# Kernel tuning notes

Hardware: AMD Instinct MI355X
Metric: run time of the kernel (lower is better)

## Reference

```python
import jax, jax.numpy as jnp
import numpy as np

B, LR_DIM, G_DIM, K, D, T = 256, 1024, 512, 64, 256, 8
GRID = jnp.linspace(-4.0, 4.0, 41)  # registered buffer in torch module


def _mu_bell(x, c, a_bell, b_bell):
    # generalized bell membership, clamp(a,b) >= 1e-3 as in torch
    a = jnp.maximum(a_bell, 1e-3)
    b = jnp.maximum(b_bell, 1e-3)
    return 1.0 / (1.0 + jnp.abs((x - c) / a) ** (2.0 * b))


def _mu_s(x, a, b):
    eps = 1e-12
    a2 = jnp.minimum(a, b)
    b2 = jnp.maximum(a, b)
    mid = (a2 + b2) * 0.5
    up = 2.0 * ((x - a2) / (b2 - a2 + eps)) ** 2
    dn = 1.0 - 2.0 * ((b2 - x) / (b2 - a2 + eps)) ** 2
    y = jnp.where((x > a2) & (x <= mid), up, jnp.zeros_like(x))
    y = jnp.where((x > mid) & (x <= b2), dn, y)
    return jnp.where(x > b2, jnp.ones_like(x), y)


def _fuzzify(x, a_bell, b_bell):
    # x: (B,d) -> (B,2d)
    xs = 4.0 * jnp.tanh(x / 4.0)
    xb = _mu_bell(xs, 0.0, a_bell, b_bell)
    xS = _mu_s(xs, -1.0, 1.0)
    return jnp.concatenate([xb, xS], axis=-1)


def _defuzzify(rt, a_bell, b_bell):
    # rt: (B,2d) -> centroid (B,d)
    d = rt.shape[1] // 2
    rb, rs = rt[:, :d], rt[:, d:]
    g = GRID[None, None, :]                      # (1,1,G)
    c_b = 4.0 * jnp.tanh(rb)[..., None]          # (B,d,1)
    c_s = 4.0 * jnp.tanh(rs)[..., None]
    mu_b = _mu_bell(g, c_b, a_bell, b_bell)      # (B,d,G)
    a_s = jnp.clip(c_s - 1.0, -4.0, 4.0)
    b_s = jnp.clip(c_s + 1.0, -4.0, 4.0)
    mu_s = _mu_s(g, a_s, b_s)
    cen_b = (g * mu_b).sum(-1) / (mu_b.sum(-1) + 1e-12)
    cen_s = (g * mu_s).sum(-1) / (mu_s.sum(-1) + 1e-12)
    return 0.5 * cen_b + 0.5 * cen_s


def _forward(wsi_lr, genomics, FT, W_lr, b_lr, W_g, b_g, WqI, WqG, WkI, WkG,
             WvI, WvG, mlp_W1, mlp_b1, mlp_W2, mlp_b2, Wf, bf, Wi, bi, Vf, Vi,
             a_bell, b_bell):
    scale = jnp.float32(D) ** 0.5
    lr = wsi_lr @ W_lr + b_lr                    # (B,d)
    g = genomics @ W_g + b_g
    lr_f = _fuzzify(lr, a_bell, b_bell)          # (B,2d)
    g_f = _fuzzify(g, a_bell, b_bell)
    QI = lr_f @ WqI                              # (B,d), loop-invariant
    QG = g_f @ WqG
    Ft0 = jnp.broadcast_to(FT[None], (wsi_lr.shape[0],) + FT.shape)  # (B,K,d)

    def step(Ft, _):
        sI = jnp.einsum('bd,bkd->bk', QI, Ft @ WkI) / scale
        sG = jnp.einsum('bd,bkd->bk', QG, Ft @ WkG) / scale
        rtI = jnp.einsum('bk,bke->be', jax.nn.softmax(sI, axis=-1), Ft @ WvI)  # (B,2d)
        rtG = jnp.einsum('bk,bke->be', jax.nn.softmax(sG, axis=-1), Ft @ WvG)
        r = 0.5 * _defuzzify(rtI, a_bell, b_bell) + 0.5 * _defuzzify(rtG, a_bell, b_bell)
        rb = jnp.broadcast_to(r[:, None, :], Ft.shape)              # (B,K,d)
        x = Ft + rb
        F_tilde = jax.nn.gelu(x @ mlp_W1 + mlp_b1, approximate=False) @ mlp_W2 + mlp_b2 + x
        f_gate = jax.nn.sigmoid(rb @ Wf + bf + jnp.tanh(Ft @ Vf))
        i_gate = jax.nn.sigmoid(rb @ Wi + bi + jnp.tanh(Ft @ Vi))
        Ft_new = f_gate * Ft + i_gate * jnp.tanh(F_tilde)
        return Ft_new, Ft_new

    _, steps = jax.lax.scan(step, Ft0, None, length=T)
    # torch stores step `T-s` result at index s-1: list index 0 holds the LAST
    # computed state, index T-1 the first -> reverse chronological order
    return steps[::-1]  # (T,B,K,d)


def setup_inputs() -> dict:
    key = jax.random.key(0)
    ks = jax.random.split(key, 20)

    def rn(k, shape, scale):
        return jax.random.normal(k, shape, dtype=jnp.float32) * scale

    z = lambda *s: jnp.zeros(s, jnp.float32)
    return dict(
        wsi_lr=rn(ks[0], (B, LR_DIM), 1.0),
        genomics=rn(ks[1], (B, G_DIM), 1.0),
        FT=rn(ks[2], (K, D), 0.02),
        W_lr=rn(ks[3], (LR_DIM, D), LR_DIM ** -0.5), b_lr=z(D),
        W_g=rn(ks[4], (G_DIM, D), G_DIM ** -0.5), b_g=z(D),
        WqI=rn(ks[5], (2 * D, D), (2 * D) ** -0.5),
        WqG=rn(ks[6], (2 * D, D), (2 * D) ** -0.5),
        WkI=rn(ks[7], (D, D), D ** -0.5),
        WkG=rn(ks[8], (D, D), D ** -0.5),
        WvI=rn(ks[9], (D, 2 * D), D ** -0.5),
        WvG=rn(ks[10], (D, 2 * D), D ** -0.5),
        mlp_W1=rn(ks[11], (D, 2 * D), D ** -0.5), mlp_b1=z(2 * D),
        mlp_W2=rn(ks[12], (2 * D, D), (2 * D) ** -0.5), mlp_b2=z(D),
        Wf=rn(ks[13], (D, D), D ** -0.5), bf=z(D),
        Wi=rn(ks[14], (D, D), D ** -0.5), bi=z(D),
        Vf=rn(ks[15], (D, D), D ** -0.5),
        Vi=rn(ks[16], (D, D), D ** -0.5),
        a_bell=jnp.float32(1.0),
        b_bell=jnp.float32(2.0),
    )


def reference(wsi_lr, genomics, FT, W_lr, b_lr, W_g, b_g, WqI, WqG, WkI, WkG,
              WvI, WvG, mlp_W1, mlp_b1, mlp_W2, mlp_b2, Wf, bf, Wi, bi, Vf, Vi,
              a_bell, b_bell):
    return _forward(wsi_lr, genomics, FT, W_lr, b_lr, W_g, b_g, WqI, WqG, WkI,
                    WkG, WvI, WvG, mlp_W1, mlp_b1, mlp_W2, mlp_b2, Wf, bf, Wi,
                    bi, Vf, Vi, a_bell, b_bell)
```

## Files before the change

### kernel.cpp

```cpp
#include <hip/hip_runtime.h>
#include <hip/hip_bf16.h>

#define B_    256
#define K_    64
#define D_    256
#define T_    8
#define NROW  (B_*K_)

typedef short short8v __attribute__((ext_vector_type(8)));
typedef float f32x4  __attribute__((ext_vector_type(4)));

__device__ __forceinline__ float fexp2(float x) { return __builtin_amdgcn_exp2f(x); }
__device__ __forceinline__ float flog2(float x) { return __builtin_amdgcn_logf(x); }

__device__ __forceinline__ float sigmoid_f(float x) {
  return 1.f / (1.f + fexp2(x * -1.4426950408889634f));
}
__device__ __forceinline__ float tanh_fast(float x) {
  float xc = fminf(fmaxf(x, -30.f), 30.f);
  float t = fexp2(xc * 2.8853900817779268f);
  return (t - 1.f) / (t + 1.f);
}
__device__ __forceinline__ float gelu_f(float x) {
  return 0.5f * x * (1.f + erff(x * 0.70710678118654752440f));
// ... 9 lines not shown
  float mid = 0.5f * (a2 + b2);
  float inv = 1.f / (b2 - a2 + 1e-12f);
  if (x > b2)  return 1.f;
  if (x > mid) { float u = (b2 - x) * inv; return 1.f - 2.f * u * u; }
  if (x > a2)  { float u = (x - a2) * inv; return 2.f * u * u; }
  return 0.f;
}
__device__ __forceinline__ float pow_abs(float z, float e2b) {
  return fexp2(e2b * flog2(fabsf(z)));
}
__device__ __forceinline__ float defuzz_one(float rb_, float rs_, float ab, float bb) {
  float e2b = 2.f * bb;
  float inv_ab = 1.f / ab;
  float cb = 4.f * tanh_fast(rb_);
  float num = 0.f, den = 0.f;
  #pragma unroll
  for (int j = 0; j < 41; ++j) {
    float gj = -4.f + 0.2f * (float)j;
    float mu = 1.f / (1.f + pow_abs((gj - cb) * inv_ab, e2b));
    num += gj * mu; den += mu;
  }
  float cenb = num / (den + 1e-12f);
  float cs = 4.f * tanh_fast(rs_);
  float as_ = fminf(fmaxf(cs - 1.f, -4.f), 4.f);
  float bs_ = fminf(fmaxf(cs + 1.f, -4.f), 4.f);
  num = 0.f; den = 0.f;
  {
    float mid = 0.5f * (as_ + bs_);
    float inv = 1.f / (bs_ - as_ + 1e-12f);
    #pragma unroll
    for (int j = 0; j < 41; ++j) {
      float gj = -4.f + 0.2f * (float)j;
      float mu;
      if (gj > bs_)      mu = 1.f;
      else if (gj > mid) { float u = (bs_ - gj) * inv; mu = 1.f - 2.f * u * u; }
      else if (gj > as_) { float u = (gj - as_) * inv; mu = 2.f * u * u; }
      else               mu = 0.f;
      num += gj * mu; den += mu;
    }
  }
  float cens = num / (den + 1e-12f);
  return 0.5f * cenb + 0.5f * cens;
}

__global__ __launch_bounds__(256) void k_convert(
    const float* __restrict__ W1, const float* __restrict__ Vf, const float* __restrict__ Vi,
    const float* __restrict__ W2, const float* __restrict__ FT,
    const float* __restrict__ WkI, const float* __restrict__ WkG,
    const float* __restrict__ WvI, const float* __restrict__ WvG,
    const float* __restrict__ Wf,  const float* __restrict__ Wi,
    unsigned short* __restrict__ B1t, unsigned short* __restrict__ W2t,
    unsigned short* __restrict__ FTbf,
    float* __restrict__ WkIt, float* __restrict__ WkGt,
    unsigned short* __restrict__ Wv2, unsigned short* __restrict__ WB)
{
  int idx = blockIdx.x * 256 + threadIdx.x;
  if (idx < 262144) {
    int n = idx >> 8, k = idx & 255;
    float v = (n < 512) ? W1[(size_t)k*512 + n]
            : (n < 768) ? Vf[(size_t)k*256 + (n-512)]
                        : Vi[(size_t)k*256 + (n-768)];
    B1t[idx] = f2bf(v);
  } else if (idx < 393216) {
    int j = idx - 262144;
    int n = j >> 9, k = j & 511;
    W2t[j] = f2bf(W2[(size_t)k*256 + n]);
  } else if (idx < 409600) {
    int j = idx - 393216;
    FTbf[j] = f2bf(FT[j]);
  } else if (idx < 475136) {
    int j = idx - 409600;
    int k = j >> 8, n = j & 255;
    WkIt[j] = WkI[(size_t)n*256 + k];
  } else if (idx < 540672) {
    int j = idx - 475136;
    int k = j >> 8, n = j & 255;
    WkGt[j] = WkG[(size_t)n*256 + k];
  } else if (idx < 802816) {
    int j = idx - 540672;
    int d = j >> 10, c = j & 1023;
    float v = (c < 512) ? WvI[(size_t)d*512 + c] : WvG[(size_t)d*512 + (c-512)];
    Wv2[j] = f2bf(v);
  } else if (idx < 1064960) {
    int j = idx - 802816;
    int d = j >> 10, c = j & 1023;
    float v = (c < 512) ? W1[(size_t)d*512 + c]
            : (c < 768) ? Wf[(size_t)d*256 + (c-512)]
                        : Wi[(size_t)d*256 + (c-768)];
    WB[j] = f2bf(v);
  }
}

__global__ __launch_bounds__(256) void k_pre_lin(
    const float* __restrict__ wsi, const float* __restrict__ gen,
    const float* __restrict__ W_lr, const float* __restrict__ b_lr,
    const float* __restrict__ W_g,  const float* __restrict__ b_g,
    const float* __restrict__ a_p,  const float* __restrict__ b_p,
    float* __restrict__ lrf, float* __restrict__ gf)
{
  int g_ix = blockIdx.x;
  int half = g_ix >> 4, tile = g_ix & 15;
  int bx = tile & 3, by = tile >> 2;
  int n0 = bx * 64, m0 = by * 64;
  const float* A    = half ? gen  : wsi;
  const float* Bm   = half ? W_g  : W_lr;
  const float* bias = half ? b_g  : b_lr;
  float* outp       = half ? gf   : lrf;
  int KK            = half ? 512  : 1024;
  float ab = fmaxf(a_p[0], 0.001f), bb = fmaxf(b_p[0], 0.001f);
  float e2b = 2.f * bb, inv_ab = 1.f / ab;

  __shared__ float As[16][64];
  __shared__ float Bs[16][64];
  int tid = threadIdx.x, tx = tid & 15, ty = tid >> 4;
  float acc[4][4] = {};
  int am = tid >> 2, ak = (tid & 3) * 4;
  int bk = tid >> 4, bn = (tid & 15) * 4;
  const float* arow = A + (size_t)(m0 + am) * KK;
  for (int k0 = 0; k0 < KK; k0 += 16) {
    float4 av = *(const float4*)(arow + k0 + ak);
    As[ak+0][am] = av.x; As[ak+1][am] = av.y; As[ak+2][am] = av.z; As[ak+3][am] = av.w;
    *(float4*)&Bs[bk][bn] = *(const float4*)(Bm + (size_t)(k0 + bk) * 256 + n0 + bn);
    __syncthreads();
    #pragma unroll
    for (int kk = 0; kk < 16; ++kk) {
      float a0 = As[kk][ty*4+0], a1 = As[kk][ty*4+1], a2 = As[kk][ty*4+2], a3 = As[kk][ty*4+3];
      float b0 = Bs[kk][tx*4+0], b1 = Bs[kk][tx*4+1], b2 = Bs[kk][tx*4+2], b3 = Bs[kk][tx*4+3];
      acc[0][0]=fmaf(a0,b0,acc[0][0]); acc[0][1]=fmaf(a0,b1,acc[0][1]); acc[0][2]=fmaf(a0,b2,acc[0][2]); acc[0][3]=fmaf(a0,b3,acc[0][3]);
      acc[1][0]=fmaf(a1,b0,acc[1][0]); acc[1][1]=fmaf(a1,b1,acc[1][1]); acc[1][2]=fmaf(a1,b2,acc[1][2]); acc[1][3]=fmaf(a1,b3,acc[1][3]);
      acc[2][0]=fmaf(a2,b0,acc[2][0]); acc[2][1]=fmaf(a2,b1,acc[2][1]); acc[2][2]=fmaf(a2,b2,acc[2][2]); acc[2][3]=fmaf(a2,b3,acc[2][3]);
      acc[3][0]=fmaf(a3,b0,acc[3][0]); acc[3][1]=fmaf(a3,b1,acc[3][1]); acc[3][2]=fmaf(a3,b2,acc[3][2]); acc[3][3]=fmaf(a3,b3,acc[3][3]);
    }
    __syncthreads();
  }
  #pragma unroll
  for (int i = 0; i < 4; ++i) {
    int row = m0 + ty*4 + i;
    #pragma unroll
    for (int j = 0; j < 4; ++j) {
      int col = n0 + tx*4 + j;
      float v = acc[i][j] + bias[col];
      float xs = 4.f * tanh_fast(v * 0.25f);
// ... 39 lines not shown
    }
    __syncthreads();
  }
  #pragma unroll
  for (int i = 0; i < 4; ++i) {
    float4 v = make_float4(acc[i][0], acc[i][1], acc[i][2], acc[i][3]);
    *(float4*)(outp + (size_t)(m0 + ty*4 + i) * 256 + n0 + tx*4) = v;
  }
}

__global__ __launch_bounds__(256) void k_pre_qp(
    const float* __restrict__ QI, const float* __restrict__ QG,
    const float* __restrict__ WkIt, const float* __restrict__ WkGt,
    float* __restrict__ qIp, float* __restrict__ qGp)
{
  int g_ix = blockIdx.x;
  int half = g_ix >> 4, tile = g_ix & 15;
  int bx = tile & 3, by = tile >> 2;
  int n0 = bx * 64, m0 = by * 64;
  const float* A  = half ? QG   : QI;
  const float* Bm = half ? WkGt : WkIt;
  float* outp     = half ? qGp  : qIp;

  __shared__ float As[16][64];
  __shared__ float Bs[16][64];
  int tid = threadIdx.x, tx = tid & 15, ty = tid >> 4;
  float acc[4][4] = {};
  int am = tid >> 2, ak = (tid & 3) * 4;
  int bk = tid >> 4, bn = (tid & 15) * 4;
  const float* arow = A + (size_t)(m0 + am) * 256;
  for (int k0 = 0; k0 < 256; k0 += 16) {
    float4 av = *(const float4*)(arow + k0 + ak);
    As[ak+0][am] = av.x; As[ak+1][am] = av.y; As[ak+2][am] = av.z; As[ak+3][am] = av.w;
    *(float4*)&Bs[bk][bn] = *(const float4*)(Bm + (size_t)(k0 + bk) * 256 + n0 + bn);
    __syncthreads();
    #pragma unroll
    for (int kk = 0; kk < 16; ++kk) {
      float a0 = As[kk][ty*4+0], a1 = As[kk][ty*4+1], a2 = As[kk][ty*4+2], a3 = As[kk][ty*4+3];
      float b0 = Bs[kk][tx*4+0], b1 = Bs[kk][tx*4+1], b2 = Bs[kk][tx*4+2], b3 = Bs[kk][tx*4+3];
      acc[0][0]=fmaf(a0,b0,acc[0][0]); acc[0][1]=fmaf(a0,b1,acc[0][1]); acc[0][2]=fmaf(a0,b2,acc[0][2]); acc[0][3]=fmaf(a0,b3,acc[0][3]);
      acc[1][0]=fmaf(a1,b0,acc[1][0]); acc[1][1]=fmaf(a1,b1,acc[1][1]); acc[1][2]=fmaf(a1,b2,acc[1][2]); acc[1][3]=fmaf(a1,b3,acc[1][3]);
      acc[2][0]=fmaf(a2,b0,acc[2][0]); acc[2][1]=fmaf(a2,b1,acc[2][1]); acc[2][2]=fmaf(a2,b2,acc[2][2]); acc[2][3]=fmaf(a2,b3,acc[2][3]);
      acc[3][0]=fmaf(a3,b0,acc[3][0]); acc[3][1]=fmaf(a3,b1,acc[3][1]); acc[3][2]=fmaf(a3,b2,acc[3][2]); acc[3][3]=fmaf(a3,b3,acc[3][3]);
    }
    __syncthreads();
  }
  #pragma unroll
  for (int i = 0; i < 4; ++i) {
    float4 v = make_float4(acc[i][0], acc[i][1], acc[i][2], acc[i][3]);
    *(float4*)(outp + (size_t)(m0 + ty*4 + i) * 256 + n0 + tx*4) = v;
  }
}

__global__ __launch_bounds__(512) void k_scan(
    const unsigned short* __restrict__ FTbf, const float* __restrict__ FTf,
    const float* __restrict__ qIp, const float* __restrict__ qGp,
    const unsigned short* __restrict__ Wv2, const unsigned short* __restrict__ WB,
    const float* __restrict__ b1, const float* __restrict__ bfv,
    const float* __restrict__ biv, const float* __restrict__ b2,
    const unsigned short* __restrict__ B1t, const unsigned short* __restrict__ W2t,
    const float* __restrict__ a_p, const float* __restrict__ b_p,
    unsigned short* __restrict__ Gf, unsigned short* __restrict__ Gi,
    float* __restrict__ out)
{
  __shared__ __align__(16) short Fs[64*264];
  __shared__ __align__(16) short Bstage[64*264];
  __shared__ __align__(16) short Wstage[256*72];
  __shared__ __align__(16) short A2ch[64*72];
  __shared__ float qv[512];
  __shared__ float red[512];
  __shared__ float prl[128];
  __shared__ float ftb[512];
  __shared__ float rL[256];
  __shared__ float rWall[1024];

  int b = blockIdx.x, tid = threadIdx.x;
  int w = tid >> 6, lane = tid & 63, lr = lane & 15, lh = lane >> 4;
  int rg = w & 3, cg = w >> 2;
  float ab = fmaxf(a_p[0], 0.001f), bb = fmaxf(b_p[0], 0.001f);

  #pragma unroll
  for (int p = 0; p < 4; ++p) {
    int idx = (p*512 + tid) * 8;
    int row = idx >> 8, col = idx & 255;
    *(float4*)&Fs[row*264 + col] = *(const float4*)&FTbf[idx];
  }
  qv[tid] = (tid < 256) ? qIp[(size_t)b*256 + tid] : qGp[(size_t)b*256 + tid - 256];
  __syncthreads();

  const float* Fprev = nullptr;
  for (int st = 0; st < T_; ++st) {
    float* Fout = out + (size_t)(7 - st) * NROW * 256;

    {
      int which = tid >> 8, tt = tid & 255, k = tt & 63, part = tt >> 6;
      const unsigned int* frow = (const unsigned int*)&Fs[k*264 + part*64];
      const float* q0 = qv + which*256 + part*64;
      float s0 = 0.f;
      #pragma unroll
      for (int d2 = 0; d2 < 32; ++d2) {
        unsigned int pr = frow[d2];
        float f0 = __uint_as_float(pr << 16);
        float f1 = __uint_as_float(pr & 0xffff0000u);
        s0 = fmaf(f1, q0[2*d2+1], fmaf(f0, q0[2*d2], s0));
      }
      red[which*256 + tt] = s0;
    }
    __syncthreads();
    if (tid < 128) {
      int which = tid >> 6, kk = tid & 63;
      const float* rp = red + which*256;
      float s = (rp[kk] + rp[64+kk] + rp[128+kk] + rp[192+kk]) * (1.f/16.f);
      float m = s;
      for (int off = 32; off; off >>= 1) m = fmaxf(m, __shfl_xor(m, off, 64));
      float e = fexp2((s - m) * 1.4426950408889634f);
      float sum = e;
      for (int off = 32; off; off >>= 1) sum += __shfl_xor(sum, off, 64);
      prl[which*64 + kk] = e / sum;
    }
    __syncthreads();
    {
      int which = tid >> 8, tt = tid & 255;
      const float* pp = prl + which*64;
      float f0 = 0.f;
      #pragma unroll 8
      for (int kk = 0; kk < 64; ++kk)
        f0 = fmaf(pp[kk], bfss((unsigned short)Fs[kk*264 + tt]), f0);
      ftb[which*256 + tt] = f0;
    }
    __syncthreads();
    {
      int half = tid >> 8, tt = tid & 255;
      const float* fb = ftb + half*256;
      const unsigned short* wv = Wv2 + half*512 + tt;
      float a0 = 0.f, a1 = 0.f;
      #pragma unroll 4
      for (int d = 0; d < 256; ++d) {
        float fv = fb[d];
        a0 = fmaf(fv, bfss(wv[(size_t)d*1024]),       a0);
        a1 = fmaf(fv, bfss(wv[(size_t)d*1024 + 256]), a1);
      }
      red[half*256 + tt] = defuzz_one(a0, a1, ab, bb);
    }
    __syncthreads();
    if (tid < 256) rL[tid] = 0.5f * (red[tid] + red[256 + tid]);
    __syncthreads();
    {
      float w0 = 0.f, w1 = 0.f;
      const unsigned short* wb0 = WB + tid;
      #pragma unroll 4
      for (int d = 0; d < 256; ++d) {
        float rv = rL[d];
        w0 = fmaf(rv, bfss(wb0[(size_t)d*1024]),       w0);
        w1 = fmaf(rv, bfss(wb0[(size_t)d*1024 + 512]), w1);
      }
      rWall[tid]       = w0 + b1[tid];
      rWall[512 + tid] = w1 + ((tid < 256) ? bfv[tid] : biv[tid - 256]);
    }
    __syncthreads();

    for (int c = 8; c < 16; ++c) {
      #pragma unroll
      for (int p = 0; p < 4; ++p) {
        int idx = (p*512 + tid) * 8;
        int row = idx >> 8, col = idx & 255;
        *(float4*)&Bstage[row*264 + col] = *(const float4*)&B1t[(size_t)c*16384 + idx];
      }
      __syncthreads();
      #pragma unroll
      for (int f = 0; f < 2; ++f) {
        f32x4 acc = {0.f,0.f,0.f,0.f};
        int nb = cg*32 + f*16;
        #pragma unroll
        for (int ks = 0; ks < 8; ++ks) {
          short8v av = *(const short8v*)&Fs[(rg*16 + lr)*264 + ks*32 + lh*8];
          short8v bv = *(const short8v*)&Bstage[(nb + lr)*264 + ks*32 + lh*8];
          acc = __builtin_amdgcn_mfma_f32_16x16x32_bf16(av, bv, acc, 0, 0, 0);
        }
        int gc = c*64 + nb + lr;
        float add = rWall[gc];
        int cc = gc - 512;
        #pragma unroll
        for (int r = 0; r < 4; ++r) {
          int row = b*64 + rg*16 + lh*4 + r;
          unsigned short val = f2bf(sigmoid_f(add + tanh_fast(acc[r])));
          if (cc < 256) Gf[(size_t)row*256 + cc]       = val;
          else          Gi[(size_t)row*256 + cc - 256] = val;
        }
      }
      __syncthreads();
    }

    f32x4 O[8];
    #pragma unroll
    for (int nn = 0; nn < 8; ++nn) { O[nn][0]=0.f; O[nn][1]=0.f; O[nn][2]=0.f; O[nn][3]=0.f; }
    for (int c = 0; c < 8; ++c) {
      #pragma unroll
      for (int p = 0; p < 4; ++p) {
        int idx = (p*512 + tid) * 8;
        int row = idx >> 8, col = idx & 255;
        *(float4*)&Bstage[row*264 + col] = *(const float4*)&B1t[(size_t)c*16384 + idx];
      }
      #pragma unroll
      for (int p = 0; p < 4; ++p) {
        int idx = (p*512 + tid) * 8;
        int n = idx >> 6, kk = idx & 63;
        *(float4*)&Wstage[n*72 + kk] = *(const float4*)&W2t[(size_t)n*512 + c*64 + kk];
      }
      __syncthreads();
      #pragma unroll
      for (int f = 0; f < 2; ++f) {
        f32x4 acc = {0.f,0.f,0.f,0.f};
        int nb = cg*32 + f*16;
        #pragma unroll
        for (int ks = 0; ks < 8; ++ks) {
          short8v av = *(const short8v*)&Fs[(rg*16 + lr)*264 + ks*32 + lh*8];
          short8v bv = *(const short8v*)&Bstage[(nb + lr)*264 + ks*32 + lh*8];
          acc = __builtin_amdgcn_mfma_f32_16x16x32_bf16(av, bv, acc, 0, 0, 0);
        }
        int gc = c*64 + nb + lr;
        float add = rWall[gc];
        #pragma unroll
        for (int r = 0; r < 4; ++r)
          A2ch[(rg*16 + lh*4 + r)*72 + nb + lr] = f2bf(gelu_f(acc[r] + add));
      }
      __syncthreads();
      #pragma unroll
      for (int ks2 = 0; ks2 < 2; ++ks2) {
        short8v av = *(const short8v*)&A2ch[(rg*16 + lr)*72 + ks2*32 + lh*8];
        #pragma unroll
        for (int nn = 0; nn < 8; ++nn) {
          short8v bv = *(const short8v*)&Wstage[(cg*128 + nn*16 + lr)*72 + ks2*32 + lh*8];
          O[nn] = __builtin_amdgcn_mfma_f32_16x16x32_bf16(av, bv, O[nn], 0, 0, 0);
        }
      }
      __syncthreads();
    }

    #pragma unroll
    for (int nn = 0; nn < 8; ++nn) {
      int col = cg*128 + nn*16 + lr;
      float b2c = b2[col], rv = rL[col];
      #pragma unroll
      for (int r = 0; r < 4; ++r) {
        int rowl = rg*16 + lh*4 + r;
        int row = b*64 + rowl;
        float Ftv = (st == 0) ? FTf[rowl*256 + col] : Fprev[(size_t)row*256 + col];
        float ftld = O[nn][r] + b2c + Ftv + rv;
        float fg = bfss(Gf[(size_t)row*256 + col]);
        float ig = bfss(Gi[(size_t)row*256 + col]);
        float ov = fg * Ftv + ig * tanh_fast(ftld);
        Fout[(size_t)row*256 + col] = ov;
        Fs[rowl*264 + col] = f2bf(ov);
      }
    }
    Fprev = Fout;
    __syncthreads();
  }
}

extern "C" void kernel_launch(void* const* d_in, const int* in_sizes, int n_in,
                              void* d_out, int out_size, void* d_ws, size_t ws_size,
                              hipStream_t stream)
{
  (void)in_sizes; (void)n_in; (void)out_size; (void)ws_size;
  const float* wsi  = (const float*)d_in[0];
  const float* gen  = (const float*)d_in[1];
  const float* FT   = (const float*)d_in[2];
  const float* W_lr = (const float*)d_in[3];
  const float* b_lr = (const float*)d_in[4];
  const float* W_g  = (const float*)d_in[5];
  const float* b_g  = (const float*)d_in[6];
  const float* WqI  = (const float*)d_in[7];
  const float* WqG  = (const float*)d_in[8];
  const float* WkI  = (const float*)d_in[9];
  const float* WkG  = (const float*)d_in[10];
  const float* WvI  = (const float*)d_in[11];
  const float* WvG  = (const float*)d_in[12];
  const float* W1   = (const float*)d_in[13];
  const float* b1   = (const float*)d_in[14];
  const float* W2   = (const float*)d_in[15];
  const float* b2   = (const float*)d_in[16];
  const float* Wf   = (const float*)d_in[17];
  const float* bf   = (const float*)d_in[18];
  const float* Wi   = (const float*)d_in[19];
  const float* bi   = (const float*)d_in[20];
  const float* Vf   = (const float*)d_in[21];
  const float* Vi   = (const float*)d_in[22];
  const float* a_p  = (const float*)d_in[23];
  const float* b_p  = (const float*)d_in[24];

  float* out = (float*)d_out;
  float* ws  = (float*)d_ws;
  float* qIp   = ws;
  float* qGp   = qIp   + 65536;
  float* lrf   = qGp   + 65536;
  float* gf    = lrf   + 131072;
  float* QI    = gf    + 131072;
  float* QG    = QI    + 65536;
  float* WkIt  = QG    + 65536;
  float* WkGt  = WkIt  + 65536;
  unsigned short* Gfb  = (unsigned short*)(WkGt + 65536);
  unsigned short* Gib  = Gfb  + 4194304;
  unsigned short* FTbf = Gib  + 4194304;
  unsigned short* B1t  = FTbf + 16384;
  unsigned short* W2t  = B1t  + 262144;
  unsigned short* Wv2  = W2t  + 131072;
  unsigned short* WB   = Wv2  + 262144;

  k_convert<<<4160, 256, 0, stream>>>(W1, Vf, Vi, W2, FT, WkI, WkG, WvI, WvG, Wf, Wi,
                                      B1t, W2t, FTbf, WkIt, WkGt, Wv2, WB);
  k_pre_lin<<<32, 256, 0, stream>>>(wsi, gen, W_lr, b_lr, W_g, b_g, a_p, b_p, lrf, gf);
  k_pre_q<<<32, 256, 0, stream>>>(lrf, gf, WqI, WqG, QI, QG);
  k_pre_qp<<<32, 256, 0, stream>>>(QI, QG, WkIt, WkGt, qIp, qGp);

  k_scan<<<256, 512, 0, stream>>>(FTbf, FT, qIp, qGp, Wv2, WB,
                                  b1, bf, bi, b2, B1t, W2t, a_p, b_p,
                                  Gfb, Gib, out);
}
```

Measured before the change: 870.3 us.

## Move scan matvecs onto MFMA with split-bf16 and drop LDS weight staging

The per-step score dot products and the Wv/WB matrix-vector products in the scan kernel now run on bf16 MFMA instead of scalar FMA loops. The vector operands and the weights are split into hi/lo bf16 pairs so the products keep near-fp32 accuracy. The B1t/W2t operands are read straight from global memory instead of being staged through shared memory, which removes several barriers and shrinks LDS use so more blocks can be resident (launch bounds ask for 4 per CU). The costs are wasted MFMA lanes (most columns or rows are zero or discarded), three MFMAs per split-precision product, and uncoalesced global fragment loads that now depend on L2 hits.

```diff
diff --git a/kernel.cpp b/kernel.cpp
--- a/kernel.cpp
+++ b/kernel.cpp
@@ -85,7 +85,8 @@
     unsigned short* __restrict__ B1t, unsigned short* __restrict__ W2t,
     unsigned short* __restrict__ FTbf,
     float* __restrict__ WkIt, float* __restrict__ WkGt,
-    unsigned short* __restrict__ Wv2, unsigned short* __restrict__ WB)
+    unsigned short* __restrict__ Wv2tH, unsigned short* __restrict__ Wv2tL,
+    unsigned short* __restrict__ WBtH,  unsigned short* __restrict__ WBtL)
 {
   int idx = blockIdx.x * 256 + threadIdx.x;
   if (idx < 262144) {
@@ -111,16 +112,20 @@
     WkGt[j] = WkG[(size_t)n*256 + k];
   } else if (idx < 802816) {
     int j = idx - 540672;
-    int d = j >> 10, c = j & 1023;
-    float v = (c < 512) ? WvI[(size_t)d*512 + c] : WvG[(size_t)d*512 + (c-512)];
-    Wv2[j] = f2bf(v);
+    int n = j >> 8, d = j & 255;
+    float v = (n < 512) ? WvI[(size_t)d*512 + n] : WvG[(size_t)d*512 + (n-512)];
+    unsigned short hi = f2bf(v);
+    Wv2tH[j] = hi;
+    Wv2tL[j] = f2bf(v - bfss(hi));
   } else if (idx < 1064960) {
     int j = idx - 802816;
-    int d = j >> 10, c = j & 1023;
-    float v = (c < 512) ? W1[(size_t)d*512 + c]
-            : (c < 768) ? Wf[(size_t)d*256 + (c-512)]
-                        : Wi[(size_t)d*256 + (c-768)];
-    WB[j] = f2bf(v);
+    int n = j >> 8, d = j & 255;
+    float v = (n < 512) ? W1[(size_t)d*512 + n]
+            : (n < 768) ? Wf[(size_t)d*256 + (n-512)]
+                        : Wi[(size_t)d*256 + (n-768)];
+    unsigned short hi = f2bf(v);
+    WBtH[j] = hi;
+    WBtL[j] = f2bf(v - bfss(hi));
   }
 }
 
@@ -266,10 +271,11 @@
   }
 }
 
-__global__ __launch_bounds__(512) void k_scan(
+__global__ __launch_bounds__(512, 4) void k_scan(
     const unsigned short* __restrict__ FTbf, const float* __restrict__ FTf,
     const float* __restrict__ qIp, const float* __restrict__ qGp,
-    const unsigned short* __restrict__ Wv2, const unsigned short* __restrict__ WB,
+    const unsigned short* __restrict__ Wv2tH, const unsigned short* __restrict__ Wv2tL,
+    const unsigned short* __restrict__ WBtH,  const unsigned short* __restrict__ WBtL,
     const float* __restrict__ b1, const float* __restrict__ bfv,
     const float* __restrict__ biv, const float* __restrict__ b2,
     const unsigned short* __restrict__ B1t, const unsigned short* __restrict__ W2t,
@@ -278,20 +284,24 @@
     float* __restrict__ out)
 {
   __shared__ __align__(16) short Fs[64*264];
-  __shared__ __align__(16) short Bstage[64*264];
-  __shared__ __align__(16) short Wstage[256*72];
   __shared__ __align__(16) short A2ch[64*72];
-  __shared__ float qv[512];
+  __shared__ __align__(16) short qpack[4*256];
+  __shared__ __align__(16) short ftbhH[512];
+  __shared__ __align__(16) short ftbhL[512];
+  __shared__ __align__(16) short rLhH[256];
+  __shared__ __align__(16) short rLhL[256];
+  __shared__ float sctmp[4*64];
   __shared__ float red[512];
   __shared__ float prl[128];
-  __shared__ float ftb[512];
   __shared__ float rL[256];
+  __shared__ float rtbuf[1024];
   __shared__ float rWall[1024];
 
   int b = blockIdx.x, tid = threadIdx.x;
   int w = tid >> 6, lane = tid & 63, lr = lane & 15, lh = lane >> 4;
   int rg = w & 3, cg = w >> 2;
   float ab = fmaxf(a_p[0], 0.001f), bb = fmaxf(b_p[0], 0.001f);
+  short8v zfrag = {0,0,0,0,0,0,0,0};
 
   #pragma unroll
   for (int p = 0; p < 4; ++p) {
@@ -299,32 +309,37 @@
     int row = idx >> 8, col = idx & 255;
     *(float4*)&Fs[row*264 + col] = *(const float4*)&FTbf[idx];
   }
-  qv[tid] = (tid < 256) ? qIp[(size_t)b*256 + tid] : qGp[(size_t)b*256 + tid - 256];
+  {
+    int which = tid >> 8, tt = tid & 255;
+    float v = which ? qGp[(size_t)b*256 + tt] : qIp[(size_t)b*256 + tt];
+    unsigned short hi = f2bf(v);
+    qpack[which*256 + tt]       = hi;
+    qpack[(which+2)*256 + tt]   = f2bf(v - bfss(hi));
+  }
   __syncthreads();
 
   const float* Fprev = nullptr;
   for (int st = 0; st < T_; ++st) {
     float* Fout = out + (size_t)(7 - st) * NROW * 256;
 
-    {
-      int which = tid >> 8, tt = tid & 255, k = tt & 63, part = tt >> 6;
-      const unsigned int* frow = (const unsigned int*)&Fs[k*264 + part*64];
-      const float* q0 = qv + which*256 + part*64;
-      float s0 = 0.f;
-      #pragma unroll
-      for (int d2 = 0; d2 < 32; ++d2) {
-        unsigned int pr = frow[d2];
-        float f0 = __uint_as_float(pr << 16);
-        float f1 = __uint_as_float(pr & 0xffff0000u);
-        s0 = fmaf(f1, q0[2*d2+1], fmaf(f0, q0[2*d2], s0));
-      }
-      red[which*256 + tt] = s0;
+    if (w < 4) {
+      f32x4 acc = {0.f,0.f,0.f,0.f};
+      #pragma unroll
+      for (int ks = 0; ks < 8; ++ks) {
+        short8v av = *(const short8v*)&Fs[(rg*16 + lr)*264 + ks*32 + lh*8];
+        short8v bq = (lr < 4) ? *(const short8v*)&qpack[lr*256 + ks*32 + lh*8] : zfrag;
+        acc = __builtin_amdgcn_mfma_f32_16x16x32_bf16(av, bq, acc, 0, 0, 0);
+      }
+      if (lr < 4) {
+        #pragma unroll
+        for (int r = 0; r < 4; ++r)
+          sctmp[lr*64 + rg*16 + lh*4 + r] = acc[r];
+      }
     }
     __syncthreads();
     if (tid < 128) {
       int which = tid >> 6, kk = tid & 63;
-      const float* rp = red + which*256;
-      float s = (rp[kk] + rp[64+kk] + rp[128+kk] + rp[192+kk]) * (1.f/16.f);
+      float s = (sctmp[which*64 + kk] + sctmp[(which+2)*64 + kk]) * (1.f/16.f);
       float m = s;
       for (int off = 32; off; off >>= 1) m = fmaxf(m, __shfl_xor(m, off, 64));
       float e = fexp2((s - m) * 1.4426950408889634f);
@@ -340,47 +355,67 @@
       #pragma unroll 8
       for (int kk = 0; kk < 64; ++kk)
         f0 = fmaf(pp[kk], bfss((unsigned short)Fs[kk*264 + tt]), f0);
-      ftb[which*256 + tt] = f0;
+      unsigned short hi = f2bf(f0);
+      ftbhH[which*256 + tt] = hi;
+      ftbhL[which*256 + tt] = f2bf(f0 - bfss(hi));
+    }
+    __syncthreads();
+    #pragma unroll
+    for (int i = 0; i < 8; ++i) {
+      int n0 = (w*8 + i) * 16;
+      int aoff = (n0 < 512) ? 0 : 256;
+      f32x4 acc = {0.f,0.f,0.f,0.f};
+      #pragma unroll
+      for (int ks = 0; ks < 8; ++ks) {
+        short8v ah = *(const short8v*)&ftbhH[aoff + ks*32 + lh*8];
+        short8v al = *(const short8v*)&ftbhL[aoff + ks*32 + lh*8];
+        short8v bh = *(const short8v*)&Wv2tH[(size_t)(n0 + lr)*256 + ks*32 + lh*8];
+        short8v bl = *(const short8v*)&Wv2tL[(size_t)(n0 + lr)*256 + ks*32 + lh*8];
+        acc = __builtin_amdgcn_mfma_f32_16x16x32_bf16(ah, bh, acc, 0, 0, 0);
+        acc = __builtin_amdgcn_mfma_f32_16x16x32_bf16(al, bh, acc, 0, 0, 0);
+        acc = __builtin_amdgcn_mfma_f32_16x16x32_bf16(ah, bl, acc, 0, 0, 0);
+      }
+      if (lh == 0) rtbuf[n0 + lr] = acc[0];
     }
     __syncthreads();
     {
       int half = tid >> 8, tt = tid & 255;
-      const float* fb = ftb + half*256;
-      const unsigned short* wv = Wv2 + half*512 + tt;
-      float a0 = 0.f, a1 = 0.f;
-      #pragma unroll 4
-      for (int d = 0; d < 256; ++d) {
-        float fv = fb[d];
-        a0 = fmaf(fv, bfss(wv[(size_t)d*1024]),       a0);
-        a1 = fmaf(fv, bfss(wv[(size_t)d*1024 + 256]), a1);
-      }
-      red[half*256 + tt] = defuzz_one(a0, a1, ab, bb);
-    }
-    __syncthreads();
-    if (tid < 256) rL[tid] = 0.5f * (red[tid] + red[256 + tid]);
+      red[half*256 + tt] = defuzz_one(rtbuf[half*512 + tt], rtbuf[half*512 + 256 + tt], ab, bb);
+    }
+    __syncthreads();
+    if (tid < 256) {
+      float rv = 0.5f * (red[tid] + red[256 + tid]);
+      rL[tid] = rv;
+      unsigned short hi = f2bf(rv);
+      rLhH[tid] = hi;
+      rLhL[tid] = f2bf(rv - bfss(hi));
+    }
+    __syncthreads();
+    #pragma unroll
+    for (int i = 0; i < 8; ++i) {
+      int n0 = (w*8 + i) * 16;
+      f32x4 acc = {0.f,0.f,0.f,0.f};
+      #pragma unroll
+      for (int ks = 0; ks < 8; ++ks) {
+        short8v ah = *(const short8v*)&rLhH[ks*32 + lh*8];
+        short8v al = *(const short8v*)&rLhL[ks*32 + lh*8];
+        short8v bh = *(const short8v*)&WBtH[(size_t)(n0 + lr)*256 + ks*32 + lh*8];
+        short8v bl = *(const short8v*)&WBtL[(size_t)(n0 + lr)*256 + ks*32 + lh*8];
+        acc = __builtin_amdgcn_mfma_f32_16x16x32_bf16(ah, bh, acc, 0, 0, 0);
+        acc = __builtin_amdgcn_mfma_f32_16x16x32_bf16(al, bh, acc, 0, 0, 0);
+        acc = __builtin_amdgcn_mfma_f32_16x16x32_bf16(ah, bl, acc, 0, 0, 0);
+      }
+      if (lh == 0) rtbuf[n0 + lr] = acc[0];
+    }
     __syncthreads();
     {
-      float w0 = 0.f, w1 = 0.f;
-      const unsigned short* wb0 = WB + tid;
-      #pragma unroll 4
-      for (int d = 0; d < 256; ++d) {
-        float rv = rL[d];
-        w0 = fmaf(rv, bfss(wb0[(size_t)d*1024]),       w0);
-        w1 = fmaf(rv, bfss(wb0[(size_t)d*1024 + 512]), w1);
-      }
-      rWall[tid]       = w0 + b1[tid];
-      rWall[512 + tid] = w1 + ((tid < 256) ? bfv[tid] : biv[tid - 256]);
+      rWall[tid]       = rtbuf[tid] + b1[tid];
+      int tt = tid & 255;
+      rWall[512 + tid] = rtbuf[512 + tid] + ((tid < 256) ? bfv[tt] : biv[tt]);
     }
     __syncthreads();
 
     for (int c = 8; c < 16; ++c) {
-      #pragma unroll
-      for (int p = 0; p < 4; ++p) {
-        int idx = (p*512 + tid) * 8;
-        int row = idx >> 8, col = idx & 255;
-        *(float4*)&Bstage[row*264 + col] = *(const float4*)&B1t[(size_t)c*16384 + idx];
-      }
-      __syncthreads();
       #pragma unroll
       for (int f = 0; f < 2; ++f) {
         f32x4 acc = {0.f,0.f,0.f,0.f};
@@ -388,7 +423,7 @@
         #pragma unroll
         for (int ks = 0; ks < 8; ++ks) {
           short8v av = *(const short8v*)&Fs[(rg*16 + lr)*264 + ks*32 + lh*8];
-          short8v bv = *(const short8v*)&Bstage[(nb + lr)*264 + ks*32 + lh*8];
+          short8v bv = *(const short8v*)&B1t[(size_t)(c*64 + nb + lr)*256 + ks*32 + lh*8];
           acc = __builtin_amdgcn_mfma_f32_16x16x32_bf16(av, bv, acc, 0, 0, 0);
         }
         int gc = c*64 + nb + lr;
@@ -402,26 +437,12 @@
           else          Gi[(size_t)row*256 + cc - 256] = val;
         }
       }
-      __syncthreads();
     }
 
     f32x4 O[8];
     #pragma unroll
     for (int nn = 0; nn < 8; ++nn) { O[nn][0]=0.f; O[nn][1]=0.f; O[nn][2]=0.f; O[nn][3]=0.f; }
     for (int c = 0; c < 8; ++c) {
-      #pragma unroll
-      for (int p = 0; p < 4; ++p) {
-        int idx = (p*512 + tid) * 8;
-        int row = idx >> 8, col = idx & 255;
-        *(float4*)&Bstage[row*264 + col] = *(const float4*)&B1t[(size_t)c*16384 + idx];
-      }
-      #pragma unroll
-      for (int p = 0; p < 4; ++p) {
-        int idx = (p*512 + tid) * 8;
-        int n = idx >> 6, kk = idx & 63;
-        *(float4*)&Wstage[n*72 + kk] = *(const float4*)&W2t[(size_t)n*512 + c*64 + kk];
-      }
-      __syncthreads();
       #pragma unroll
       for (int f = 0; f < 2; ++f) {
         f32x4 acc = {0.f,0.f,0.f,0.f};
@@ -429,7 +450,7 @@
         #pragma unroll
         for (int ks = 0; ks < 8; ++ks) {
           short8v av = *(const short8v*)&Fs[(rg*16 + lr)*264 + ks*32 + lh*8];
-          short8v bv = *(const short8v*)&Bstage[(nb + lr)*264 + ks*32 + lh*8];
+          short8v bv = *(const short8v*)&B1t[(size_t)(c*64 + nb + lr)*256 + ks*32 + lh*8];
           acc = __builtin_amdgcn_mfma_f32_16x16x32_bf16(av, bv, acc, 0, 0, 0);
         }
         int gc = c*64 + nb + lr;
@@ -444,8 +465,8 @@
         short8v av = *(const short8v*)&A2ch[(rg*16 + lr)*72 + ks2*32 + lh*8];
         #pragma unroll
         for (int nn = 0; nn < 8; ++nn) {
-          short8v bv = *(const short8v*)&Wstage[(cg*128 + nn*16 + lr)*72 + ks2*32 + lh*8];
-          O[nn] = __builtin_amdgcn_mfma_f32_16x16x32_bf16(av, bv, O[nn], 0, 0, 0);
+          short8v bw = *(const short8v*)&W2t[(size_t)(cg*128 + nn*16 + lr)*512 + c*64 + ks2*32 + lh*8];
+          O[nn] = __builtin_amdgcn_mfma_f32_16x16x32_bf16(av, bw, O[nn], 0, 0, 0);
         }
       }
       __syncthreads();
@@ -514,21 +535,24 @@
   float* QG    = QI    + 65536;
   float* WkIt  = QG    + 65536;
   float* WkGt  = WkIt  + 65536;
-  unsigned short* Gfb  = (unsigned short*)(WkGt + 65536);
-  unsigned short* Gib  = Gfb  + 4194304;
-  unsigned short* FTbf = Gib  + 4194304;
-  unsigned short* B1t  = FTbf + 16384;
-  unsigned short* W2t  = B1t  + 262144;
-  unsigned short* Wv2  = W2t  + 131072;
-  unsigned short* WB   = Wv2  + 262144;
+  unsigned short* Gfb   = (unsigned short*)(WkGt + 65536);
+  unsigned short* Gib   = Gfb   + 4194304;
+  unsigned short* FTbf  = Gib   + 4194304;
+  unsigned short* B1t   = FTbf  + 16384;
+  unsigned short* W2t   = B1t   + 262144;
+  unsigned short* Wv2tH = W2t   + 131072;
+  unsigned short* Wv2tL = Wv2tH + 262144;
+  unsigned short* WBtH  = Wv2tL + 262144;
+  unsigned short* WBtL  = WBtH  + 262144;
 
   k_convert<<<4160, 256, 0, stream>>>(W1, Vf, Vi, W2, FT, WkI, WkG, WvI, WvG, Wf, Wi,
-                                      B1t, W2t, FTbf, WkIt, WkGt, Wv2, WB);
+                                      B1t, W2t, FTbf, WkIt, WkGt,
+                                      Wv2tH, Wv2tL, WBtH, WBtL);
   k_pre_lin<<<32, 256, 0, stream>>>(wsi, gen, W_lr, b_lr, W_g, b_g, a_p, b_p, lrf, gf);
   k_pre_q<<<32, 256, 0, stream>>>(lrf, gf, WqI, WqG, QI, QG);
   k_pre_qp<<<32, 256, 0, stream>>>(QI, QG, WkIt, WkGt, qIp, qGp);
 
-  k_scan<<<256, 512, 0, stream>>>(FTbf, FT, qIp, qGp, Wv2, WB,
+  k_scan<<<256, 512, 0, stream>>>(FTbf, FT, qIp, qGp, Wv2tH, Wv2tL, WBtH, WBtL,
                                   b1, bf, bi, b2, B1t, W2t, a_p, b_p,
                                   Gfb, Gib, out);
 }
```

Result: slower. 3.165 ms (+263.7%).

## Keep forget/input gates in registers instead of global scratch; use fp32 Wv/WB weights

Applied to the files above, without the earlier changes.

Gate computation is remapped so that each wave computes the forget and input gate tiles matching the output tile it later owns. The bf16 results are packed into registers rather than written to and reread from global Gf/Gi buffers. This removes a global round-trip per step, at the cost of more registers and some load imbalance, since only half the waves compute gates in each chunk. The Wv and WB matrices are also stored as fp32, which doubles their read traffic but avoids the bf16 conversion.

```diff
diff --git a/kernel.cpp b/kernel.cpp
--- a/kernel.cpp
+++ b/kernel.cpp
@@ -85,7 +85,7 @@
     unsigned short* __restrict__ B1t, unsigned short* __restrict__ W2t,
     unsigned short* __restrict__ FTbf,
     float* __restrict__ WkIt, float* __restrict__ WkGt,
-    unsigned short* __restrict__ Wv2, unsigned short* __restrict__ WB)
+    float* __restrict__ Wv2f, float* __restrict__ WBf)
 {
   int idx = blockIdx.x * 256 + threadIdx.x;
   if (idx < 262144) {
@@ -112,15 +112,13 @@
   } else if (idx < 802816) {
     int j = idx - 540672;
     int d = j >> 10, c = j & 1023;
-    float v = (c < 512) ? WvI[(size_t)d*512 + c] : WvG[(size_t)d*512 + (c-512)];
-    Wv2[j] = f2bf(v);
+    Wv2f[j] = (c < 512) ? WvI[(size_t)d*512 + c] : WvG[(size_t)d*512 + (c-512)];
   } else if (idx < 1064960) {
     int j = idx - 802816;
     int d = j >> 10, c = j & 1023;
-    float v = (c < 512) ? W1[(size_t)d*512 + c]
-            : (c < 768) ? Wf[(size_t)d*256 + (c-512)]
-                        : Wi[(size_t)d*256 + (c-768)];
-    WB[j] = f2bf(v);
+    WBf[j] = (c < 512) ? W1[(size_t)d*512 + c]
+           : (c < 768) ? Wf[(size_t)d*256 + (c-512)]
+                       : Wi[(size_t)d*256 + (c-768)];
   }
 }
 
@@ -269,12 +267,11 @@
 __global__ __launch_bounds__(512) void k_scan(
     const unsigned short* __restrict__ FTbf, const float* __restrict__ FTf,
     const float* __restrict__ qIp, const float* __restrict__ qGp,
-    const unsigned short* __restrict__ Wv2, const unsigned short* __restrict__ WB,
+    const float* __restrict__ Wv2f, const float* __restrict__ WBf,
     const float* __restrict__ b1, const float* __restrict__ bfv,
     const float* __restrict__ biv, const float* __restrict__ b2,
     const unsigned short* __restrict__ B1t, const unsigned short* __restrict__ W2t,
     const float* __restrict__ a_p, const float* __restrict__ b_p,
-    unsigned short* __restrict__ Gf, unsigned short* __restrict__ Gi,
     float* __restrict__ out)
 {
   __shared__ __align__(16) short Fs[64*264];
@@ -346,13 +343,13 @@
     {
       int half = tid >> 8, tt = tid & 255;
       const float* fb = ftb + half*256;
-      const unsigned short* wv = Wv2 + half*512 + tt;
+      const float* wvp = Wv2f + half*512 + tt;
       float a0 = 0.f, a1 = 0.f;
       #pragma unroll 4
       for (int d = 0; d < 256; ++d) {
         float fv = fb[d];
-        a0 = fmaf(fv, bfss(wv[(size_t)d*1024]),       a0);
-        a1 = fmaf(fv, bfss(wv[(size_t)d*1024 + 256]), a1);
+        a0 = fmaf(fv, wvp[(size_t)d*1024],       a0);
+        a1 = fmaf(fv, wvp[(size_t)d*1024 + 256], a1);
       }
       red[half*256 + tt] = defuzz_one(a0, a1, ab, bb);
     }
@@ -361,18 +358,21 @@
     __syncthreads();
     {
       float w0 = 0.f, w1 = 0.f;
-      const unsigned short* wb0 = WB + tid;
+      const float* wbp = WBf + tid;
       #pragma unroll 4
       for (int d = 0; d < 256; ++d) {
         float rv = rL[d];
-        w0 = fmaf(rv, bfss(wb0[(size_t)d*1024]),       w0);
-        w1 = fmaf(rv, bfss(wb0[(size_t)d*1024 + 512]), w1);
+        w0 = fmaf(rv, wbp[(size_t)d*1024],       w0);
+        w1 = fmaf(rv, wbp[(size_t)d*1024 + 512], w1);
       }
       rWall[tid]       = w0 + b1[tid];
-      rWall[512 + tid] = w1 + ((tid < 256) ? bfv[tid] : biv[tid - 256]);
-    }
-    __syncthreads();
-
+      int tt = tid & 255;
+      rWall[512 + tid] = w1 + ((tid < 256) ? bfv[tt] : biv[tt]);
+    }
+    __syncthreads();
+
+    unsigned int ufg[8][2] = {}, uig[8][2] = {};
+    #pragma unroll
     for (int c = 8; c < 16; ++c) {
       #pragma unroll
       for (int p = 0; p < 4; ++p) {
@@ -381,25 +381,30 @@
         *(float4*)&Bstage[row*264 + col] = *(const float4*)&B1t[(size_t)c*16384 + idx];
       }
       __syncthreads();
-      #pragma unroll
-      for (int f = 0; f < 2; ++f) {
-        f32x4 acc = {0.f,0.f,0.f,0.f};
-        int nb = cg*32 + f*16;
+      const int crel = c - 8;
+      const int isGi = crel >= 4;
+      const int cq = crel & 3;
+      const int nnbase = (cq & 1) * 4;
+      if ((cq >> 1) == cg) {
         #pragma unroll
-        for (int ks = 0; ks < 8; ++ks) {
-          short8v av = *(const short8v*)&Fs[(rg*16 + lr)*264 + ks*32 + lh*8];
-          short8v bv = *(const short8v*)&Bstage[(nb + lr)*264 + ks*32 + lh*8];
-          acc = __builtin_amdgcn_mfma_f32_16x16x32_bf16(av, bv, acc, 0, 0, 0);
-        }
-        int gc = c*64 + nb + lr;
-        float add = rWall[gc];
-        int cc = gc - 512;
-        #pragma unroll
-        for (int r = 0; r < 4; ++r) {
-          int row = b*64 + rg*16 + lh*4 + r;
-          unsigned short val = f2bf(sigmoid_f(add + tanh_fast(acc[r])));
-          if (cc < 256) Gf[(size_t)row*256 + cc]       = val;
-          else          Gi[(size_t)row*256 + cc - 256] = val;
+        for (int j = 0; j < 4; ++j) {
+          f32x4 acc = {0.f,0.f,0.f,0.f};
+          #pragma unroll
+          for (int ks = 0; ks < 8; ++ks) {
+            short8v av = *(const short8v*)&Fs[(rg*16 + lr)*264 + ks*32 + lh*8];
+            short8v bv = *(const short8v*)&Bstage[(j*16 + lr)*264 + ks*32 + lh*8];
+            acc = __builtin_amdgcn_mfma_f32_16x16x32_bf16(av, bv, acc, 0, 0, 0);
+          }
+          int col = c*64 + j*16 + lr;
+          float add = rWall[col];
+          unsigned short v0 = f2bf(sigmoid_f(add + tanh_fast(acc[0])));
+          unsigned short v1 = f2bf(sigmoid_f(add + tanh_fast(acc[1])));
+          unsigned short v2 = f2bf(sigmoid_f(add + tanh_fast(acc[2])));
+          unsigned short v3 = f2bf(sigmoid_f(add + tanh_fast(acc[3])));
+          unsigned int p0 = (((unsigned int)v1) << 16) | v0;
+          unsigned int p1 = (((unsigned int)v3) << 16) | v2;
+          if (isGi) { uig[nnbase+j][0] = p0; uig[nnbase+j][1] = p1; }
+          else      { ufg[nnbase+j][0] = p0; ufg[nnbase+j][1] = p1; }
         }
       }
       __syncthreads();
@@ -444,8 +449,8 @@
         short8v av = *(const short8v*)&A2ch[(rg*16 + lr)*72 + ks2*32 + lh*8];
         #pragma unroll
         for (int nn = 0; nn < 8; ++nn) {
-          short8v bv = *(const short8v*)&Wstage[(cg*128 + nn*16 + lr)*72 + ks2*32 + lh*8];
-          O[nn] = __builtin_amdgcn_mfma_f32_16x16x32_bf16(av, bv, O[nn], 0, 0, 0);
+          short8v bw = *(const short8v*)&Wstage[(cg*128 + nn*16 + lr)*72 + ks2*32 + lh*8];
+          O[nn] = __builtin_amdgcn_mfma_f32_16x16x32_bf16(av, bw, O[nn], 0, 0, 0);
         }
       }
       __syncthreads();
@@ -461,8 +466,9 @@
         int row = b*64 + rowl;
         float Ftv = (st == 0) ? FTf[rowl*256 + col] : Fprev[(size_t)row*256 + col];
         float ftld = O[nn][r] + b2c + Ftv + rv;
-        float fg = bfss(Gf[(size_t)row*256 + col]);
-        float ig = bfss(Gi[(size_t)row*256 + col]);
+        unsigned int pf_ = ufg[nn][r>>1], pi_ = uig[nn][r>>1];
+        float fg = bfss((unsigned short)((r & 1) ? (pf_ >> 16) : (pf_ & 0xffffu)));
+        float ig = bfss((unsigned short)((r & 1) ? (pi_ >> 16) : (pi_ & 0xffffu)));
         float ov = fg * Ftv + ig * tanh_fast(ftld);
         Fout[(size_t)row*256 + col] = ov;
         Fs[rowl*264 + col] = f2bf(ov);
@@ -514,21 +520,18 @@
   float* QG    = QI    + 65536;
   float* WkIt  = QG    + 65536;
   float* WkGt  = WkIt  + 65536;
-  unsigned short* Gfb  = (unsigned short*)(WkGt + 65536);
-  unsigned short* Gib  = Gfb  + 4194304;
-  unsigned short* FTbf = Gib  + 4194304;
+  float* Wv2f  = WkGt  + 65536;
+  float* WBf   = Wv2f  + 262144;
+  unsigned short* FTbf = (unsigned short*)(WBf + 262144);
   unsigned short* B1t  = FTbf + 16384;
   unsigned short* W2t  = B1t  + 262144;
-  unsigned short* Wv2  = W2t  + 131072;
-  unsigned short* WB   = Wv2  + 262144;
 
   k_convert<<<4160, 256, 0, stream>>>(W1, Vf, Vi, W2, FT, WkI, WkG, WvI, WvG, Wf, Wi,
-                                      B1t, W2t, FTbf, WkIt, WkGt, Wv2, WB);
+                                      B1t, W2t, FTbf, WkIt, WkGt, Wv2f, WBf);
   k_pre_lin<<<32, 256, 0, stream>>>(wsi, gen, W_lr, b_lr, W_g, b_g, a_p, b_p, lrf, gf);
   k_pre_q<<<32, 256, 0, stream>>>(lrf, gf, WqI, WqG, QI, QG);
   k_pre_qp<<<32, 256, 0, stream>>>(QI, QG, WkIt, WkGt, qIp, qGp);
 
-  k_scan<<<256, 512, 0, stream>>>(FTbf, FT, qIp, qGp, Wv2, WB,
-                                  b1, bf, bi, b2, B1t, W2t, a_p, b_p,
-                                  Gfb, Gib, out);
-}
+  k_scan<<<256, 512, 0, stream>>>(FTbf, FT, qIp, qGp, Wv2f, WBf,
+                                  b1, bf, bi, b2, B1t, W2t, a_p, b_p, out);
+}
```

New measurement: 1.275 ms. 1.46x slower.

## Keep forget/input gates in registers and prefetch weight chunks into registers

Applied to the files above, without the earlier changes.

The gate values Gf/Gi used to be written to global memory in bf16 and read back in the epilogue. They are now staged through a shared-memory chunk buffer, and the owning warps pack them into registers, so the global gate buffers go away. The weight chunks for B1t and W2t are also software-prefetched into registers one chunk ahead, so the global loads overlap with the MFMA work. In exchange there is more register pressure (32 packed gate words plus 8 prefetch float4s), which could hurt occupancy or cause spills.

```diff
diff --git a/kernel.cpp b/kernel.cpp
--- a/kernel.cpp
+++ b/kernel.cpp
@@ -274,13 +274,12 @@
     const float* __restrict__ biv, const float* __restrict__ b2,
     const unsigned short* __restrict__ B1t, const unsigned short* __restrict__ W2t,
     const float* __restrict__ a_p, const float* __restrict__ b_p,
-    unsigned short* __restrict__ Gf, unsigned short* __restrict__ Gi,
     float* __restrict__ out)
 {
   __shared__ __align__(16) short Fs[64*264];
   __shared__ __align__(16) short Bstage[64*264];
   __shared__ __align__(16) short Wstage[256*72];
-  __shared__ __align__(16) short A2ch[64*72];
+  __shared__ __align__(16) short XCh[64*72];
   __shared__ float qv[512];
   __shared__ float red[512];
   __shared__ float prl[128];
@@ -369,18 +368,95 @@
         w1 = fmaf(rv, bfss(wb0[(size_t)d*1024 + 512]), w1);
       }
       rWall[tid]       = w0 + b1[tid];
-      rWall[512 + tid] = w1 + ((tid < 256) ? bfv[tid] : biv[tid - 256]);
-    }
-    __syncthreads();
-
+      int tt = tid & 255;
+      rWall[512 + tid] = w1 + ((tid < 256) ? bfv[tt] : biv[tt]);
+    }
+    __syncthreads();
+
+    unsigned int ufg[8][2] = {}, uig[8][2] = {};
+    float4 pfB[4];
+    #pragma unroll
+    for (int p = 0; p < 4; ++p)
+      pfB[p] = *(const float4*)&B1t[(size_t)8*16384 + (p*512 + tid)*8];
+    #pragma unroll
     for (int c = 8; c < 16; ++c) {
       #pragma unroll
       for (int p = 0; p < 4; ++p) {
         int idx = (p*512 + tid) * 8;
         int row = idx >> 8, col = idx & 255;
-        *(float4*)&Bstage[row*264 + col] = *(const float4*)&B1t[(size_t)c*16384 + idx];
+        *(float4*)&Bstage[row*264 + col] = pfB[p];
       }
       __syncthreads();
+      if (c < 15) {
+        #pragma unroll
+        for (int p = 0; p < 4; ++p)
+          pfB[p] = *(const float4*)&B1t[(size_t)(c+1)*16384 + (p*512 + tid)*8];
+      }
+      #pragma unroll
+      for (int f = 0; f < 2; ++f) {
+        f32x4 acc = {0.f,0.f,0.f,0.f};
+        int nb = cg*32 + f*16;
+        #pragma unroll
+        for (int ks = 0; ks < 8; ++ks) {
+          short8v av = *(const short8v*)&Fs[(rg*16 + lr)*264 + ks*32 + lh*8];
+          short8v bv = *(const short8v*)&Bstage[(nb + lr)*264 + ks*32 + lh*8];
+          acc = __builtin_amdgcn_mfma_f32_16x16x32_bf16(av, bv, acc, 0, 0, 0);
+        }
+        int colL = nb + lr;
+        float add = rWall[c*64 + colL];
+        #pragma unroll
+        for (int r = 0; r < 4; ++r)
+          XCh[(rg*16 + lh*4 + r)*72 + colL] = f2bf(sigmoid_f(add + tanh_fast(acc[r])));
+      }
+      __syncthreads();
+      const int crel = c - 8;
+      const int isGi = crel >= 4;
+      const int cq = crel & 3;
+      if ((cq >> 1) == cg) {
+        const int nnb = (cq & 1) * 4;
+        #pragma unroll
+        for (int m = 0; m < 4; ++m) {
+          #pragma unroll
+          for (int rr = 0; rr < 2; ++rr) {
+            unsigned short g0 = (unsigned short)XCh[(rg*16 + lh*4 + 2*rr    )*72 + m*16 + lr];
+            unsigned short g1 = (unsigned short)XCh[(rg*16 + lh*4 + 2*rr + 1)*72 + m*16 + lr];
+            unsigned int pk = (((unsigned int)g1) << 16) | g0;
+            if (isGi) uig[nnb+m][rr] = pk; else ufg[nnb+m][rr] = pk;
+          }
+        }
+      }
+    }
+
+    f32x4 O[8];
+    #pragma unroll
+    for (int nn = 0; nn < 8; ++nn) { O[nn][0]=0.f; O[nn][1]=0.f; O[nn][2]=0.f; O[nn][3]=0.f; }
+    float4 pfW[4];
+    #pragma unroll
+    for (int p = 0; p < 4; ++p) {
+      int idx = (p*512 + tid) * 8;
+      pfB[p] = *(const float4*)&B1t[idx];
+      int n = idx >> 6, kk = idx & 63;
+      pfW[p] = *(const float4*)&W2t[(size_t)n*512 + kk];
+    }
+    for (int c = 0; c < 8; ++c) {
+      #pragma unroll
+      for (int p = 0; p < 4; ++p) {
+        int idx = (p*512 + tid) * 8;
+        int row = idx >> 8, col = idx & 255;
+        *(float4*)&Bstage[row*264 + col] = pfB[p];
+        int n = idx >> 6, kk = idx & 63;
+        *(float4*)&Wstage[n*72 + kk] = pfW[p];
+      }
+      __syncthreads();
+      if (c < 7) {
+        #pragma unroll
+        for (int p = 0; p < 4; ++p) {
+          int idx = (p*512 + tid) * 8;
+          pfB[p] = *(const float4*)&B1t[(size_t)(c+1)*16384 + idx];
+          int n = idx >> 6, kk = idx & 63;
+          pfW[p] = *(const float4*)&W2t[(size_t)n*512 + (c+1)*64 + kk];
+        }
+      }
       #pragma unroll
       for (int f = 0; f < 2; ++f) {
         f32x4 acc = {0.f,0.f,0.f,0.f};
@@ -393,59 +469,18 @@
         }
         int gc = c*64 + nb + lr;
         float add = rWall[gc];
-        int cc = gc - 512;
-        #pragma unroll
-        for (int r = 0; r < 4; ++r) {
-          int row = b*64 + rg*16 + lh*4 + r;
-          unsigned short val = f2bf(sigmoid_f(add + tanh_fast(acc[r])));
-          if (cc < 256) Gf[(size_t)row*256 + cc]       = val;
-          else          Gi[(size_t)row*256 + cc - 256] = val;
-        }
+        #pragma unroll
+        for (int r = 0; r < 4; ++r)
+          XCh[(rg*16 + lh*4 + r)*72 + nb + lr] = f2bf(gelu_f(acc[r] + add));
       }
       __syncthreads();
-    }
-
-    f32x4 O[8];
-    #pragma unroll
-    for (int nn = 0; nn < 8; ++nn) { O[nn][0]=0.f; O[nn][1]=0.f; O[nn][2]=0.f; O[nn][3]=0.f; }
-    for (int c = 0; c < 8; ++c) {
-      #pragma unroll
-      for (int p = 0; p < 4; ++p) {
-        int idx = (p*512 + tid) * 8;
-        int row = idx >> 8, col = idx & 255;
-        *(float4*)&Bstage[row*264 + col] = *(const float4*)&B1t[(size_t)c*16384 + idx];
-      }
-      #pragma unroll
-      for (int p = 0; p < 4; ++p) {
-        int idx = (p*512 + tid) * 8;
-        int n = idx >> 6, kk = idx & 63;
-        *(float4*)&Wstage[n*72 + kk] = *(const float4*)&W2t[(size_t)n*512 + c*64 + kk];
-      }
-      __syncthreads();
-      #pragma unroll
-      for (int f = 0; f < 2; ++f) {
-        f32x4 acc = {0.f,0.f,0.f,0.f};
-        int nb = cg*32 + f*16;
-        #pragma unroll
-        for (int ks = 0; ks < 8; ++ks) {
-          short8v av = *(const short8v*)&Fs[(rg*16 + lr)*264 + ks*32 + lh*8];
-          short8v bv = *(const short8v*)&Bstage[(nb + lr)*264 + ks*32 + lh*8];
-          acc = __builtin_amdgcn_mfma_f32_16x16x32_bf16(av, bv, acc, 0, 0, 0);
-        }
-        int gc = c*64 + nb + lr;
-        float add = rWall[gc];
-        #pragma unroll
-        for (int r = 0; r < 4; ++r)
-          A2ch[(rg*16 + lh*4 + r)*72 + nb + lr] = f2bf(gelu_f(acc[r] + add));
-      }
-      __syncthreads();
       #pragma unroll
       for (int ks2 = 0; ks2 < 2; ++ks2) {
-        short8v av = *(const short8v*)&A2ch[(rg*16 + lr)*72 + ks2*32 + lh*8];
+        short8v av = *(const short8v*)&XCh[(rg*16 + lr)*72 + ks2*32 + lh*8];
         #pragma unroll
         for (int nn = 0; nn < 8; ++nn) {
-          short8v bv = *(const short8v*)&Wstage[(cg*128 + nn*16 + lr)*72 + ks2*32 + lh*8];
-          O[nn] = __builtin_amdgcn_mfma_f32_16x16x32_bf16(av, bv, O[nn], 0, 0, 0);
+          short8v bw = *(const short8v*)&Wstage[(cg*128 + nn*16 + lr)*72 + ks2*32 + lh*8];
+          O[nn] = __builtin_amdgcn_mfma_f32_16x16x32_bf16(av, bw, O[nn], 0, 0, 0);
         }
       }
       __syncthreads();
@@ -461,8 +496,9 @@
         int row = b*64 + rowl;
         float Ftv = (st == 0) ? FTf[rowl*256 + col] : Fprev[(size_t)row*256 + col];
         float ftld = O[nn][r] + b2c + Ftv + rv;
-        float fg = bfss(Gf[(size_t)row*256 + col]);
-        float ig = bfss(Gi[(size_t)row*256 + col]);
+        unsigned int pf_ = ufg[nn][r>>1], pi_ = uig[nn][r>>1];
+        float fg = bfss((unsigned short)((r & 1) ? (pf_ >> 16) : (pf_ & 0xffffu)));
+        float ig = bfss((unsigned short)((r & 1) ? (pi_ >> 16) : (pi_ & 0xffffu)));
         float ov = fg * Ftv + ig * tanh_fast(ftld);
         Fout[(size_t)row*256 + col] = ov;
         Fs[rowl*264 + col] = f2bf(ov);
@@ -514,9 +550,7 @@
   float* QG    = QI    + 65536;
   float* WkIt  = QG    + 65536;
   float* WkGt  = WkIt  + 65536;
-  unsigned short* Gfb  = (unsigned short*)(WkGt + 65536);
-  unsigned short* Gib  = Gfb  + 4194304;
-  unsigned short* FTbf = Gib  + 4194304;
+  unsigned short* FTbf = (unsigned short*)(WkGt + 65536);
   unsigned short* B1t  = FTbf + 16384;
   unsigned short* W2t  = B1t  + 262144;
   unsigned short* Wv2  = W2t  + 131072;
@@ -529,6 +563,5 @@
   k_pre_qp<<<32, 256, 0, stream>>>(QI, QG, WkIt, WkGt, qIp, qGp);
 
   k_scan<<<256, 512, 0, stream>>>(FTbf, FT, qIp, qGp, Wv2, WB,
-                                  b1, bf, bi, b2, B1t, W2t, a_p, b_p,
-                                  Gfb, Gib, out);
-}
+                                  b1, bf, bi, b2, B1t, W2t, a_p, b_p, out);
+}
```

Result: slower. 1.175 ms (+35.1%).
